# Performance work log

Hardware: AMD Instinct MI355X
Metric: run time of the kernel (lower is better)

## Reference

```python
import jax, jax.numpy as jnp
import numpy as np

NUM_EMB = 256
EMB_DIM = 128
COMMIT_COST = 0.25


def setup_inputs() -> dict:
    key = jax.random.key(0)
    k1, k2 = jax.random.split(key)
    z = jax.random.normal(k1, (64, EMB_DIM, 64, 64), dtype=jnp.float32)
    # codebook initialized uniform(-1/num_embeddings, 1/num_embeddings)
    emb = jax.random.uniform(k2, (NUM_EMB, EMB_DIM), dtype=jnp.float32,
                             minval=-1.0 / NUM_EMB, maxval=1.0 / NUM_EMB)
    return {"z": z, "emb": emb}


def reference(z, emb):
    B, C, H, W = z.shape
    # [B, C, H, W] -> [B*H*W, C]
    z_flat = jnp.transpose(z, (0, 2, 3, 1)).reshape(-1, C)
    # squared L2 distances to each code: ||z||^2 - 2 z.e + ||e||^2, shape [N, K]
    d = (jnp.sum(z_flat * z_flat, axis=1, keepdims=True)
         - 2.0 * jnp.einsum('nc,kc->nk', z_flat, emb)
         + jnp.sum(emb * emb, axis=1))
    idx = jnp.argmin(d, axis=1)  # [N]
    # gather codes, back to NCHW
    quantized = emb[idx].reshape(B, H, W, C)
    quantized = jnp.transpose(quantized, (0, 3, 1, 2))
    commitment_loss = COMMIT_COST * jnp.mean(
        (jax.lax.stop_gradient(quantized) - z) ** 2)
    codebook_loss = jnp.mean((quantized - jax.lax.stop_gradient(z)) ** 2)
    # straight-through estimator
    quantized_ste = z + jax.lax.stop_gradient(quantized - z)
    return (quantized_ste, idx.reshape(B, H, W), commitment_loss, codebook_loss)
```

## Files before the change

### kernel.cpp

```cpp
#include <hip/hip_runtime.h>

#define K_EMB   256
#define C_DIM   128
#define HW      4096
#define NPOS    262144
#define Q_ELEMS 33554432
#define IDX_OFF Q_ELEMS
#define LOSS_OFF (Q_ELEMS + NPOS)

#define BLKP 64
#define NTHR 512
#define TM   4
#define TN   8
#define NKG  32

#define WS_ENORM 0
#define WS_ACC   256
#define WS_EMBT  512
#define WS_NEED_FULL  ((WS_EMBT + C_DIM * K_EMB) * 4)

__global__ __launch_bounds__(K_EMB) void vq_transpose(const float* __restrict__ emb,
                                                      float* __restrict__ ws,
                                                      int use_embT) {
    const int c = blockIdx.x, k = threadIdx.x;
    if (use_embT) ws[WS_EMBT + c * K_EMB + k] = emb[k * C_DIM + c];
    if (c == 0 && k == 0) ws[WS_ACC] = 0.f;
}

__global__ __launch_bounds__(K_EMB) void vq_enorm(const float* __restrict__ emb,
                                                  float* __restrict__ ws) {
    const int k = threadIdx.x;
    const float4* __restrict__ er = reinterpret_cast<const float4*>(emb + k * C_DIM);
    float s = 0.f;
    #pragma unroll
    for (int j = 0; j < C_DIM / 4; ++j) {
        float4 v = er[j];
        s = fmaf(v.x, v.x, s);
        s = fmaf(v.y, v.y, s);
        s = fmaf(v.z, v.z, s);
        s = fmaf(v.w, v.w, s);
    }
    ws[WS_ENORM + k] = s;
}

template <int UT>
__global__ __launch_bounds__(NTHR, 4) void vq_main(const float* __restrict__ z,
                                                   const float* __restrict__ emb,
                                                   const float* __restrict__ ws,
                                                   float* __restrict__ out,
                                                   float* __restrict__ loss_acc) {
    __shared__ float zlds[C_DIM * BLKP];
    __shared__ float shz[BLKP];
    __shared__ float shen[K_EMB];
    __shared__ float shpb[NKG * BLKP];
    __shared__ unsigned int shpi[NKG * BLKP / 4];

    const int t   = threadIdx.x;
    const int pg  = t & 15;
    const int p0  = pg * 4;
    const int kg  = t >> 4;
    const int k0  = kg * TN;
    const int blk = blockIdx.x;
    const int b   = blk >> 6;
    const int hw0 = (blk & 63) * BLKP;
    const size_t zoff = (size_t)b * (C_DIM * HW) + hw0;
    const float* __restrict__ zsrc = z + zoff;

    const float* __restrict__ embT    = ws + WS_EMBT;
    const float* __restrict__ enorm_g = ws + WS_ENORM;

    {
        const float4* __restrict__ zs4 = reinterpret_cast<const float4*>(zsrc);
        float4* __restrict__ zl4 = reinterpret_cast<float4*>(zlds);
        #pragma unroll
        for (int j = 0; j < (C_DIM * BLKP / 4) / NTHR; ++j) {
            const int i4 = t + j * NTHR;
            const int c  = i4 >> 4;
            const int p4 = i4 & 15;
            zl4[i4] = zs4[(size_t)c * (HW / 4) + p4];
        }
        if (t < K_EMB) shen[t] = enorm_g[t];
    }
    __syncthreads();

    if (t < BLKP) {
        float zn = 0.f;
        #pragma unroll 8
        for (int c = 0; c < C_DIM; ++c) {
            const float zc = zlds[c * BLKP + t];
            zn = fmaf(zc, zc, zn);
        }
        shz[t] = zn;
    }

    float acc[TM][TN];
    #pragma unroll
    for (int i = 0; i < TM; ++i)
        #pragma unroll
        for (int j = 0; j < TN; ++j) acc[i][j] = 0.f;

    #pragma unroll 4
    for (int c = 0; c < C_DIM; ++c) {
        const float4 zv = *reinterpret_cast<const float4*>(&zlds[c * BLKP + p0]);
        float ev[TN];
        if (UT) {
            const float4* __restrict__ ep =
                reinterpret_cast<const float4*>(embT + c * K_EMB + k0);
            const float4 e0 = ep[0];
            const float4 e1 = ep[1];
            ev[0] = e0.x; ev[1] = e0.y; ev[2] = e0.z; ev[3] = e0.w;
            ev[4] = e1.x; ev[5] = e1.y; ev[6] = e1.z; ev[7] = e1.w;
        } else {
            #pragma unroll
            for (int j = 0; j < TN; ++j) ev[j] = emb[(k0 + j) * C_DIM + c];
        }
        const float zz[TM] = {zv.x, zv.y, zv.z, zv.w};
        #pragma unroll
        for (int i = 0; i < TM; ++i)
            #pragma unroll
            for (int j = 0; j < TN; ++j)
                acc[i][j] = fmaf(zz[i], ev[j], acc[i][j]);
    }
    __syncthreads();

    {
        float pb[TM];
        int   pi[TM];
        #pragma unroll
        for (int i = 0; i < TM; ++i) {
            const float zn = shz[p0 + i];
            float best = 3.402823466e38f;
            int   bi = 0;
            #pragma unroll
            for (int j = 0; j < TN; ++j) {
                const float d = (zn - 2.0f * acc[i][j]) + shen[k0 + j];
                if (d < best) { best = d; bi = k0 + j; }
            }
            pb[i] = best; pi[i] = bi;
        }
        *reinterpret_cast<float4*>(&shpb[kg * BLKP + p0]) =
            make_float4(pb[0], pb[1], pb[2], pb[3]);
        shpi[kg * 16 + pg] = (unsigned)(pi[0] & 255) | ((unsigned)(pi[1] & 255) << 8)
                           | ((unsigned)(pi[2] & 255) << 16) | ((unsigned)(pi[3] & 255) << 24);
    }
    __syncthreads();

    if (t < BLKP) {
        const int p = t;
        float bb = shpb[p];
        int   bi = (shpi[p >> 2] >> ((p & 3) * 8)) & 255;
        #pragma unroll 4
        for (int g = 1; g < NKG; ++g) {
            const float bq = shpb[g * BLKP + p];
            const int   iq = (shpi[g * 16 + (p >> 2)] >> ((p & 3) * 8)) & 255;
            if (bq < bb) { bb = bq; bi = iq; }
        }
        const int fin = bi;
        const int pos = blk * BLKP + p;
        __builtin_nontemporal_store((float)fin, &out[IDX_OFF + pos]);

        float lsum = 0.f;
        float* qp = out + zoff + p;
        const float4* __restrict__ er =
            reinterpret_cast<const float4*>(emb + fin * C_DIM);
        #pragma unroll 4
        for (int j = 0; j < C_DIM / 4; ++j) {
            const float4 ev = er[j];
            const int c0 = j * 4;
            const float z0 = zlds[(c0 + 0) * BLKP + p];
            const float z1 = zlds[(c0 + 1) * BLKP + p];
            const float z2 = zlds[(c0 + 2) * BLKP + p];
            const float z3 = zlds[(c0 + 3) * BLKP + p];
            const float d0 = ev.x - z0, d1 = ev.y - z1;
            const float d2 = ev.z - z2, d3 = ev.w - z3;
            lsum = fmaf(d0, d0, lsum);
            lsum = fmaf(d1, d1, lsum);
            lsum = fmaf(d2, d2, lsum);
            lsum = fmaf(d3, d3, lsum);
            __builtin_nontemporal_store(z0 + d0, &qp[(size_t)(c0 + 0) * HW]);
            __builtin_nontemporal_store(z1 + d1, &qp[(size_t)(c0 + 1) * HW]);
            __builtin_nontemporal_store(z2 + d2, &qp[(size_t)(c0 + 2) * HW]);
            __builtin_nontemporal_store(z3 + d3, &qp[(size_t)(c0 + 3) * HW]);
        }

        #pragma unroll
        for (int off = 32; off > 0; off >>= 1)
            lsum += __shfl_down(lsum, off, 64);
        if (p == 0) atomicAdd(loss_acc, lsum);
    }
}

__global__ void vq_finalize(const float* __restrict__ loss_acc,
                            float* __restrict__ out_losses) {
    float S = loss_acc[0];
    float mean = S / (float)Q_ELEMS;
    out_losses[0] = 0.25f * mean;
    out_losses[1] = mean;
}

extern "C" void kernel_launch(void* const* d_in, const int* in_sizes, int n_in,
                              void* d_out, int out_size, void* d_ws, size_t ws_size,
                              hipStream_t stream) {
    const float* z   = (const float*)d_in[0];
    const float* emb = (const float*)d_in[1];
    float* out = (float*)d_out;
    float* ws  = (float*)d_ws;

    int use_embT = (ws_size >= (size_t)WS_NEED_FULL) ? 1 : 0;

    vq_transpose<<<C_DIM, K_EMB, 0, stream>>>(emb, ws, use_embT);
    vq_enorm<<<1, K_EMB, 0, stream>>>(emb, ws);
    if (use_embT)
        vq_main<1><<<NPOS / BLKP, NTHR, 0, stream>>>(z, emb, ws, out, ws + WS_ACC);
    else
        vq_main<0><<<NPOS / BLKP, NTHR, 0, stream>>>(z, emb, ws, out, ws + WS_ACC);
    vq_finalize<<<1, 1, 0, stream>>>(ws + WS_ACC, out + LOSS_OFF);
}
```

Baseline: 456.8 us.

## Stage codebook chunks in LDS via async global-to-LDS loads, double-buffered

The main kernel now copies z and the transposed codebook into LDS with direct global-to-LDS loads. The codebook moves in double-buffered chunks of 16 channels, so each thread's inner-loop codebook reads hit LDS instead of global/L1 memory. The per-position squared norm of z is folded into the main FMA loop instead of a separate serial pass, and the two prep kernels are merged into one launch. The extra ~32KB of LDS per block lowers how many blocks fit on a CU, and more barriers are added inside the channel loop.

```diff
diff --git a/kernel.cpp b/kernel.cpp
--- a/kernel.cpp
+++ b/kernel.cpp
@@ -10,37 +10,42 @@
 
 #define BLKP 64
 #define NTHR 512
+#define NW   8
+#define CC   16
+#define NCHUNK (C_DIM / CC)
 #define TM   4
 #define TN   8
-#define NKG  32
+#define NG   32
 
 #define WS_ENORM 0
 #define WS_ACC   256
 #define WS_EMBT  512
 #define WS_NEED_FULL  ((WS_EMBT + C_DIM * K_EMB) * 4)
 
-__global__ __launch_bounds__(K_EMB) void vq_transpose(const float* __restrict__ emb,
-                                                      float* __restrict__ ws,
-                                                      int use_embT) {
+#define GLOAD16(gsrc, ldst) __builtin_amdgcn_global_load_lds(                 \
+    (const __attribute__((address_space(1))) void*)(gsrc),                    \
+    (__attribute__((address_space(3))) void*)(ldst), 16, 0, 0)
+
+__global__ __launch_bounds__(K_EMB) void vq_prep(const float* __restrict__ emb,
+                                                 float* __restrict__ ws,
+                                                 int use_embT) {
     const int c = blockIdx.x, k = threadIdx.x;
-    if (use_embT) ws[WS_EMBT + c * K_EMB + k] = emb[k * C_DIM + c];
-    if (c == 0 && k == 0) ws[WS_ACC] = 0.f;
-}
-
-__global__ __launch_bounds__(K_EMB) void vq_enorm(const float* __restrict__ emb,
-                                                  float* __restrict__ ws) {
-    const int k = threadIdx.x;
-    const float4* __restrict__ er = reinterpret_cast<const float4*>(emb + k * C_DIM);
-    float s = 0.f;
-    #pragma unroll
-    for (int j = 0; j < C_DIM / 4; ++j) {
-        float4 v = er[j];
-        s = fmaf(v.x, v.x, s);
-        s = fmaf(v.y, v.y, s);
-        s = fmaf(v.z, v.z, s);
-        s = fmaf(v.w, v.w, s);
-    }
-    ws[WS_ENORM + k] = s;
+    if (c < C_DIM) {
+        if (use_embT) ws[WS_EMBT + c * K_EMB + k] = emb[k * C_DIM + c];
+        if (c == 0 && k == 0) ws[WS_ACC] = 0.f;
+    } else {
+        const float4* __restrict__ er = reinterpret_cast<const float4*>(emb + k * C_DIM);
+        float s = 0.f;
+        #pragma unroll
+        for (int j = 0; j < C_DIM / 4; ++j) {
+            float4 v = er[j];
+            s = fmaf(v.x, v.x, s);
+            s = fmaf(v.y, v.y, s);
+            s = fmaf(v.z, v.z, s);
+            s = fmaf(v.w, v.w, s);
+        }
+        ws[WS_ENORM + k] = s;
+    }
 }
 
 template <int UT>
@@ -50,110 +55,141 @@
                                                    float* __restrict__ out,
                                                    float* __restrict__ loss_acc) {
     __shared__ float zlds[C_DIM * BLKP];
-    __shared__ float shz[BLKP];
+    __shared__ float ebuf[2][CC * K_EMB];
     __shared__ float shen[K_EMB];
-    __shared__ float shpb[NKG * BLKP];
-    __shared__ unsigned int shpi[NKG * BLKP / 4];
-
-    const int t   = threadIdx.x;
-    const int pg  = t & 15;
-    const int p0  = pg * 4;
-    const int kg  = t >> 4;
-    const int k0  = kg * TN;
-    const int blk = blockIdx.x;
-    const int b   = blk >> 6;
-    const int hw0 = (blk & 63) * BLKP;
+    __shared__ float shpb[NG * BLKP];
+    __shared__ unsigned int shpi[NG * BLKP / 4];
+
+    const int t    = threadIdx.x;
+    const int lane = t & 63;
+    const int w    = t >> 6;
+    const int pg   = lane & 15;
+    const int cg   = lane >> 4;
+    const int p0   = pg * 4;
+    const int k0   = w * 32 + cg * 8;
+    const int blk  = blockIdx.x;
+    const int b    = blk >> 6;
+    const int hw0  = (blk & 63) * BLKP;
     const size_t zoff = (size_t)b * (C_DIM * HW) + hw0;
     const float* __restrict__ zsrc = z + zoff;
 
     const float* __restrict__ embT    = ws + WS_EMBT;
     const float* __restrict__ enorm_g = ws + WS_ENORM;
 
-    {
-        const float4* __restrict__ zs4 = reinterpret_cast<const float4*>(zsrc);
-        float4* __restrict__ zl4 = reinterpret_cast<float4*>(zlds);
-        #pragma unroll
-        for (int j = 0; j < (C_DIM * BLKP / 4) / NTHR; ++j) {
-            const int i4 = t + j * NTHR;
-            const int c  = i4 >> 4;
-            const int p4 = i4 & 15;
-            zl4[i4] = zs4[(size_t)c * (HW / 4) + p4];
-        }
-        if (t < K_EMB) shen[t] = enorm_g[t];
-    }
+    #pragma unroll
+    for (int j = 0; j < 4; ++j) {
+        const int i4 = t + j * NTHR;
+        const int c  = i4 >> 4;
+        const int p4 = i4 & 15;
+        GLOAD16(zsrc + (size_t)c * HW + p4 * 4, &zlds[i4 * 4]);
+    }
+    if (UT) {
+        #pragma unroll
+        for (int s = 0; s < 2; ++s) {
+            const int i4 = t + s * NTHR;
+            GLOAD16(embT + i4 * 4, &ebuf[0][i4 * 4]);
+        }
+    }
+    if (t < K_EMB) shen[t] = enorm_g[t];
     __syncthreads();
 
-    if (t < BLKP) {
-        float zn = 0.f;
-        #pragma unroll 8
+    float acc[TM][TN];
+    float zn[TM];
+    #pragma unroll
+    for (int i = 0; i < TM; ++i) {
+        zn[i] = 0.f;
+        #pragma unroll
+        for (int j = 0; j < TN; ++j) acc[i][j] = 0.f;
+    }
+
+    if (UT) {
+        for (int ch = 0; ch < NCHUNK; ++ch) {
+            if (ch + 1 < NCHUNK) {
+                const float* __restrict__ src = embT + (ch + 1) * CC * K_EMB;
+                #pragma unroll
+                for (int s = 0; s < 2; ++s) {
+                    const int i4 = t + s * NTHR;
+                    GLOAD16(src + i4 * 4, &ebuf[(ch + 1) & 1][i4 * 4]);
+                }
+            }
+            const float* __restrict__ eb = ebuf[ch & 1];
+            const int cbase = ch * CC;
+            #pragma unroll 4
+            for (int c = 0; c < CC; ++c) {
+                const float4 zv = *reinterpret_cast<const float4*>(
+                    &zlds[(cbase + c) * BLKP + p0]);
+                const float4 e0 = *reinterpret_cast<const float4*>(
+                    &eb[c * K_EMB + k0]);
+                const float4 e1 = *reinterpret_cast<const float4*>(
+                    &eb[c * K_EMB + k0 + 4]);
+                const float zz[TM] = {zv.x, zv.y, zv.z, zv.w};
+                const float ee[TN] = {e0.x, e0.y, e0.z, e0.w,
+                                      e1.x, e1.y, e1.z, e1.w};
+                #pragma unroll
+                for (int i = 0; i < TM; ++i) {
+                    zn[i] = fmaf(zz[i], zz[i], zn[i]);
+                    #pragma unroll
+                    for (int j = 0; j < TN; ++j)
+                        acc[i][j] = fmaf(zz[i], ee[j], acc[i][j]);
+                }
+            }
+            if (ch + 1 < NCHUNK) {
+                __syncthreads();
+            }
+        }
+    } else {
+        #pragma unroll 2
         for (int c = 0; c < C_DIM; ++c) {
-            const float zc = zlds[c * BLKP + t];
-            zn = fmaf(zc, zc, zn);
-        }
-        shz[t] = zn;
-    }
-
-    float acc[TM][TN];
-    #pragma unroll
-    for (int i = 0; i < TM; ++i)
-        #pragma unroll
-        for (int j = 0; j < TN; ++j) acc[i][j] = 0.f;
-
-    #pragma unroll 4
-    for (int c = 0; c < C_DIM; ++c) {
-        const float4 zv = *reinterpret_cast<const float4*>(&zlds[c * BLKP + p0]);
-        float ev[TN];
-        if (UT) {
-            const float4* __restrict__ ep =
-                reinterpret_cast<const float4*>(embT + c * K_EMB + k0);
-            const float4 e0 = ep[0];
-            const float4 e1 = ep[1];
-            ev[0] = e0.x; ev[1] = e0.y; ev[2] = e0.z; ev[3] = e0.w;
-            ev[4] = e1.x; ev[5] = e1.y; ev[6] = e1.z; ev[7] = e1.w;
-        } else {
+            const float4 zv = *reinterpret_cast<const float4*>(&zlds[c * BLKP + p0]);
+            const float zz[TM] = {zv.x, zv.y, zv.z, zv.w};
+            float ee[TN];
             #pragma unroll
-            for (int j = 0; j < TN; ++j) ev[j] = emb[(k0 + j) * C_DIM + c];
-        }
-        const float zz[TM] = {zv.x, zv.y, zv.z, zv.w};
-        #pragma unroll
-        for (int i = 0; i < TM; ++i)
+            for (int j = 0; j < TN; ++j) ee[j] = emb[(k0 + j) * C_DIM + c];
             #pragma unroll
-            for (int j = 0; j < TN; ++j)
-                acc[i][j] = fmaf(zz[i], ev[j], acc[i][j]);
-    }
-    __syncthreads();
+            for (int i = 0; i < TM; ++i) {
+                zn[i] = fmaf(zz[i], zz[i], zn[i]);
+                #pragma unroll
+                for (int j = 0; j < TN; ++j)
+                    acc[i][j] = fmaf(zz[i], ee[j], acc[i][j]);
+            }
+        }
+    }
 
     {
         float pb[TM];
-        int   pi[TM];
+        int   pi_[TM];
         #pragma unroll
         for (int i = 0; i < TM; ++i) {
-            const float zn = shz[p0 + i];
             float best = 3.402823466e38f;
             int   bi = 0;
             #pragma unroll
             for (int j = 0; j < TN; ++j) {
-                const float d = (zn - 2.0f * acc[i][j]) + shen[k0 + j];
+                const float d = (zn[i] - 2.0f * acc[i][j]) + shen[k0 + j];
                 if (d < best) { best = d; bi = k0 + j; }
             }
-            pb[i] = best; pi[i] = bi;
-        }
-        *reinterpret_cast<float4*>(&shpb[kg * BLKP + p0]) =
+            pb[i] = best; pi_[i] = bi;
+        }
+        const int g = w * 4 + cg;
+        *reinterpret_cast<float4*>(&shpb[g * BLKP + p0]) =
             make_float4(pb[0], pb[1], pb[2], pb[3]);
-        shpi[kg * 16 + pg] = (unsigned)(pi[0] & 255) | ((unsigned)(pi[1] & 255) << 8)
-                           | ((unsigned)(pi[2] & 255) << 16) | ((unsigned)(pi[3] & 255) << 24);
+        shpi[g * 16 + pg] = (unsigned)(pi_[0] & 255)
+                          | ((unsigned)(pi_[1] & 255) << 8)
+                          | ((unsigned)(pi_[2] & 255) << 16)
+                          | ((unsigned)(pi_[3] & 255) << 24);
     }
     __syncthreads();
 
     if (t < BLKP) {
         const int p = t;
         float bb = shpb[p];
-        int   bi = (shpi[p >> 2] >> ((p & 3) * 8)) & 255;
+        int   bi = (int)((shpi[p >> 2] >> ((p & 3) * 8)) & 255u);
         #pragma unroll 4
-        for (int g = 1; g < NKG; ++g) {
+        for (int g = 1; g < NG; ++g) {
             const float bq = shpb[g * BLKP + p];
-            const int   iq = (shpi[g * 16 + (p >> 2)] >> ((p & 3) * 8)) & 255;
-            if (bq < bb) { bb = bq; bi = iq; }
+            if (bq < bb) {
+                bb = bq;
+                bi = (int)((shpi[g * 16 + (p >> 2)] >> ((p & 3) * 8)) & 255u);
+            }
         }
         const int fin = bi;
         const int pos = blk * BLKP + p;
@@ -208,8 +244,7 @@
 
     int use_embT = (ws_size >= (size_t)WS_NEED_FULL) ? 1 : 0;
 
-    vq_transpose<<<C_DIM, K_EMB, 0, stream>>>(emb, ws, use_embT);
-    vq_enorm<<<1, K_EMB, 0, stream>>>(emb, ws);
+    vq_prep<<<C_DIM + 1, K_EMB, 0, stream>>>(emb, ws, use_embT);
     if (use_embT)
         vq_main<1><<<NPOS / BLKP, NTHR, 0, stream>>>(z, emb, ws, out, ws + WS_ACC);
     else
```

After: 412.2 us. 1.11x faster.
